# Performance work log

Hardware: AMD Instinct MI355X
Metric: run time of the kernel (lower is better)

## Reference

```python
import jax, jax.numpy as jnp
import numpy as np
import math

N_HEAD = 12

def alibi_slopes(h):
    x = (2 ** 8) ** (1.0 / h)
    return jnp.array([1.0 / x ** (i + 1) for i in range(h)], dtype=jnp.float32)

def setup_inputs() -> dict:
    key = jax.random.key(0)
    k0, k1, k2 = jax.random.split(key, 3)
    B, T, C = 4, 2048, 576
    x = jax.random.normal(k0, (B, T, C), dtype=jnp.float32)
    w_qkv = jax.random.normal(k1, (3 * C, C), dtype=jnp.float32) * 0.02
    w_proj = jax.random.normal(k2, (C, C), dtype=jnp.float32) * 0.02
    return {"x": x, "w_qkv": w_qkv, "w_proj": w_proj}

def reference(x, w_qkv, w_proj):
    B, T, C = x.shape
    H = N_HEAD
    D = C // H
    qkv = x @ w_qkv.T  # [B,T,3C]
    q, k, v = jnp.split(qkv, 3, axis=2)
    q = q.reshape(B, T, H, D).transpose(0, 2, 1, 3)  # [B,H,T,D]
    k = k.reshape(B, T, H, D).transpose(0, 2, 1, 3)
    v = v.reshape(B, T, H, D).transpose(0, 2, 1, 3)
    # value residual with v1=None: v = 0.5*v + 0.5*v = v (faithful no-op)
    scale = 1.0 / math.sqrt(D)
    att = jnp.einsum('bhid,bhjd->bhij', q, k) * scale  # [B,H,T,T]
    # ALiBi bias as written: (col - row).clamp(min=0) * slope (zero on causal part)
    col = jnp.arange(T, dtype=jnp.float32)[None, :]
    row = jnp.arange(T, dtype=jnp.float32)[:, None]
    bias = jnp.maximum(col - row, 0.0)[None, :, :] * alibi_slopes(H)[:, None, None]  # [H,T,T]
    att = att + bias[None]
    causal = (jnp.arange(T)[None, :] <= jnp.arange(T)[:, None])  # [T,T] lower-tri
    att = jnp.where(causal[None, None], att, -jnp.inf)
    att = jax.nn.softmax(att, axis=-1)
    y = jnp.einsum('bhij,bhjd->bhid', att, v)  # [B,H,T,D]
    y = y.transpose(0, 2, 1, 3).reshape(B, T, C)
    return y @ w_proj.T
```

## Files before the change

### kernel.cpp

```cpp
#include <hip/hip_runtime.h>
#include <math.h>

#define Bn 4
#define Tn 2048
#define Cn 576
#define Hn 12
#define Dn 48
#define Mn (Bn*Tn)

#define QSCALE (1.4426950408889634f * 0.14433756729740643f)

typedef short  short8  __attribute__((ext_vector_type(8)));
typedef float  floatx4 __attribute__((ext_vector_type(4)));
typedef unsigned short ushort_t;
typedef unsigned short ushort8_t __attribute__((ext_vector_type(8)));

static __device__ __forceinline__ unsigned short f2bf(float f) {
    union { float f; unsigned int u; } v; v.f = f;
    unsigned int r = v.u + 0x7FFFu + ((v.u >> 16) & 1u);
    return (unsigned short)(r >> 16);
}

static __device__ __forceinline__ unsigned int pack_trunc(float a, float b) {
    union { float f; unsigned int u; } ua, ub; ua.f = a; ub.f = b;
    return (ua.u >> 16) | (ub.u & 0xFFFF0000u);
}

static __device__ __forceinline__ void gload16(void* lds, const void* g) {
    __builtin_amdgcn_global_load_lds(
        (const __attribute__((address_space(1))) void*)g,
        (__attribute__((address_space(3))) void*)lds, 16, 0, 0);
}

template<int N> static __device__ __forceinline__ void vmgate() {
    if constexpr (N == 0)      asm volatile("s_waitcnt vmcnt(0)" ::: "memory");
    else if constexpr (N == 4) asm volatile("s_waitcnt vmcnt(4)" ::: "memory");
    else if constexpr (N == 8) asm volatile("s_waitcnt vmcnt(8)" ::: "memory");
}
static __device__ __forceinline__ void lgk0() {
    asm volatile("s_waitcnt lgkmcnt(0)" ::: "memory");
}
static __device__ __forceinline__ void barrier_fence() {
    asm volatile("" ::: "memory");
    __builtin_amdgcn_s_barrier();
    asm volatile("" ::: "memory");
}

template<int N> static __device__ __forceinline__ void wait_vm_lg() {
    if constexpr (N == 0)
        asm volatile("s_waitcnt vmcnt(0) lgkmcnt(0)" ::: "memory");
    else if constexpr (N == 3)
        asm volatile("s_waitcnt vmcnt(3) lgkmcnt(0)" ::: "memory");
    else if constexpr (N == 6)
        asm volatile("s_waitcnt vmcnt(6) lgkmcnt(0)" ::: "memory");
    else
        static_assert(N == -12345, "unsupported waitcnt immediate");
}

__global__ __launch_bounds__(256)
void cast3(const float* __restrict__ a, ushort_t* __restrict__ oa, int na4,
           const float* __restrict__ b, ushort_t* __restrict__ ob, int nb4,
           const float* __restrict__ c, ushort_t* __restrict__ oc, int nc4,
           ushort_t* __restrict__ zb)
{
    int i = blockIdx.x * 256 + threadIdx.x;
    if (blockIdx.x == 0 && threadIdx.x < 16) {
        float4 z = (float4){0.f, 0.f, 0.f, 0.f};
        ((float4*)zb)[threadIdx.x] = z;
    }
    const float* src; ushort_t* dst; int idx;
    if (i < na4)                  { src = a; dst = oa; idx = i; }
    else if (i < na4 + nb4)       { src = b; dst = ob; idx = i - na4; }
    else if (i < na4 + nb4 + nc4) { src = c; dst = oc; idx = i - na4 - nb4; }
    else return;
    float4 v = ((const float4*)src)[idx];
    ushort4 o;
    o.x = f2bf(v.x); o.y = f2bf(v.y); o.z = f2bf(v.z); o.w = f2bf(v.w);
    ((ushort4*)dst)[idx] = o;
}

__global__ __launch_bounds__(512)
void gemm_qkv(const ushort_t* __restrict__ A, const ushort_t* __restrict__ W,
              ushort_t* __restrict__ outb)
{
    __shared__ __align__(16) ushort_t Ls[8][8192];

    const int tid  = threadIdx.x;
    const int wave = tid >> 6;
    const int lane = tid & 63;
    const int m    = lane & 15;
    const int g    = lane >> 4;
    const int wr   = wave >> 2;
    const int wn   = wave & 3;

    const int bid  = blockIdx.x;
    const int xcd  = bid & 7;
    const int slot = bid >> 3;
    const int ng   = slot % 7;
    const int mg   = xcd + 8 * (slot / 7);
    const int m0   = mg * 256;
    const int n0g  = ng * 256;

    const int srow = lane >> 2;
    const int schk = (lane & 3) * 16;
    const char* aS0 = (const char*)A + (size_t)(m0  + (wave*2+0)*16 + srow) * (Cn*2) + schk;
    const char* aS1 = (const char*)A + (size_t)(m0  + (wave*2+1)*16 + srow) * (Cn*2) + schk;
    const char* bS0 = (const char*)W + (size_t)(n0g + (wave*2+0)*16 + srow) * (Cn*2) + schk;
    const char* bS1 = (const char*)W + (size_t)(n0g + (wave*2+1)*16 + srow) * (Cn*2) + schk;

    const int aoff = (wr * 128 + m) * 64 + g * 16;
    const int boff = (wn * 64  + m) * 64 + g * 16;

    floatx4 acc[8][4];
    #pragma unroll
    for (int i = 0; i < 8; ++i)
        #pragma unroll
        for (int j = 0; j < 4; ++j)
            acc[i][j] = (floatx4){0.f, 0.f, 0.f, 0.f};

    short8 af[8], bf01[2], bf23[2];

    auto stageA = [&](int s) {
        gload16(&Ls[s][(wave*2+0)*512], aS0); aS0 += 64;
        gload16(&Ls[s][(wave*2+1)*512], aS1); aS1 += 64;
    };
    auto stageB = [&](int s) {
        gload16(&Ls[s][(wave*2+0)*512], bS0); bS0 += 64;
        gload16(&Ls[s][(wave*2+1)*512], bS1); bS1 += 64;
    };
    auto loadA = [&](int s) {
        const char* base = (const char*)&Ls[s][0] + aoff;
        #pragma unroll
        for (int mf = 0; mf < 8; ++mf) af[mf] = *(const short8*)(base + mf * 1024);
    };
    auto loadB = [&](int s, int nf0, short8 (&bf)[2]) {
        const char* base = (const char*)&Ls[s][0] + boff;
        bf[0] = *(const short8*)(base + (nf0 + 0) * 1024);
        bf[1] = *(const short8*)(base + (nf0 + 1) * 1024);
    };
    auto mfma16 = [&](short8 (&bf)[2], int nf0) {
        __builtin_amdgcn_s_setprio(1);
        #pragma unroll
        for (int mf = 0; mf < 8; ++mf) {
            acc[mf][nf0]     = __builtin_amdgcn_mfma_f32_16x16x32_bf16(af[mf], bf[0], acc[mf][nf0],     0, 0, 0);
            acc[mf][nf0 + 1] = __builtin_amdgcn_mfma_f32_16x16x32_bf16(af[mf], bf[1], acc[mf][nf0 + 1], 0, 0, 0);
        }
        __builtin_amdgcn_s_setprio(0);
    };

    stageA(0); stageB(1); stageA(2); stageB(3); stageA(4); stageB(5);
    vmgate<8>();
    barrier_fence();

    #define QKV_TILE(s0, d0, d1, d2, d3, G1m, G3m) do {                         \
        constexpr int A0 = (s0) & 7,      B0 = ((s0)+1) & 7;                    \
        constexpr int A1 = ((s0)+2) & 7,  B1 = ((s0)+3) & 7;                    \
        constexpr int S0 = ((s0)+6) & 7,  S1 = ((s0)+7) & 7;                    \
        constexpr int S2 = ((s0)+8) & 7,  S3 = ((s0)+9) & 7;                    \
        loadA(A0); loadB(B0, 0, bf01);                                          \
        if (d0) stageA(S0);                                                     \
        barrier_fence(); lgk0();                                                \
        mfma16(bf01, 0);                                                        \
        barrier_fence();                                                        \
        loadB(B0, 2, bf23);                                                     \
        if (d1) stageB(S1);                                                     \
        barrier_fence(); lgk0();                                                \
        mfma16(bf23, 2);                                                        \
        vmgate<G1m>();                                                          \
        barrier_fence();                                                        \
        loadA(A1); loadB(B1, 0, bf01);                                          \
        if (d2) stageA(S2);                                                     \
        barrier_fence(); lgk0();                                                \
        mfma16(bf01, 0);                                                        \
        barrier_fence();                                                        \
        loadB(B1, 2, bf23);                                                     \
        if (d3) stageB(S3);                                                     \
        barrier_fence(); lgk0();                                                \
        mfma16(bf23, 2);                                                        \
        vmgate<G3m>();                                                          \
        barrier_fence();                                                        \
    } while (0)

    #pragma unroll 1
    for (int tt = 0; tt < 3; ++tt) {
        QKV_TILE(0, 1, 1, 1, 1, 8, 8);
        QKV_TILE(4, 1, 1, 1, 1, 8, 8);
    }
    QKV_TILE(0, 1, 1, 1, 1, 8, 8);
    QKV_TILE(4, 1, 1, 0, 0, 8, 4);
    QKV_TILE(0, 0, 0, 0, 0, 0, -1);
    #undef QKV_TILE

    const size_t per = (size_t)Bn * Hn * Tn * Dn;
    const int b  = m0 >> 11;
    const int t0 = m0 & 2047;
    ushort_t* Lc = (ushort_t*)&Ls[0][0];

    #pragma unroll
    for (int h2 = 0; h2 < 2; ++h2) {
        const int  nbase = n0g + h2 * 128;
        const bool vmode = (nbase >= 1152);
        if ((wn >> 1) == h2) {
            if (!vmode) {
                #pragma unroll
                for (int mf = 0; mf < 8; ++mf)
                    #pragma unroll
                    for (int nf = 0; nf < 4; ++nf) {
                        const int  nfb = n0g + wn * 64 + nf * 16;
                        const float sc = (nfb < 576) ? QSCALE : 1.0f;
                        const int col = (wn & 1) * 64 + nf * 16 + m;
                        const int rb  = wr * 128 + mf * 16 + g * 4;
                        #pragma unroll
                        for (int r = 0; r < 4; ++r)
                            Lc[(rb + r) * 136 + col] = f2bf(acc[mf][nf][r] * sc);
                    }
            } else {
                #pragma unroll
                for (int mf = 0; mf < 8; ++mf)
                    #pragma unroll
                    for (int nf = 0; nf < 4; ++nf) {
                        const int col = (wn & 1) * 64 + nf * 16 + m;
                        const int rb  = wr * 128 + mf * 16 + g * 4;
                        ushort4 pk;
                        pk.x = f2bf(acc[mf][nf][0]); pk.y = f2bf(acc[mf][nf][1]);
                        pk.z = f2bf(acc[mf][nf][2]); pk.w = f2bf(acc[mf][nf][3]);
                        *(ushort4*)&Lc[col * 264 + rb] = pk;
                    }
            }
        }
        __syncthreads();
        if (!vmode) {
            #pragma unroll
            for (int it = 0; it < 8; ++it) {
                const int c   = tid + it * 512;
                const int row = c >> 4;
                const int c8  = (c & 15) * 8;
                const int n   = nbase + c8;
                const int which = (n >= 576);
                const int nn  = n - which * 576;
                const int h   = nn / 48, d = nn - h * 48;
                ushort_t* dst = outb + (size_t)which * per
                    + ((size_t)(b * Hn + h) * Tn + t0 + row) * Dn + d;
                *(ushort8_t*)dst = *(const ushort8_t*)&Lc[row * 136 + c8];
            }
        } else {
            #pragma unroll
            for (int it = 0; it < 8; ++it) {
                const int c   = tid + it * 512;
                const int col = c >> 5;
                const int rc  = (c & 31) * 8;
                const int n   = nbase + col;
                if (n < 1728) {
                    const int dd = n - 1152;
                    const int h  = dd / 48, d = dd - h * 48;
                    ushort_t* dst = outb + 2 * per
                        + ((size_t)(b * Hn + h) * Dn + d) * Tn + t0 + rc;
                    *(ushort8_t*)dst = *(const ushort8_t*)&Lc[col * 264 + rc];
                }
            }
        }
        __syncthreads();
    }
}

template<int MODE, int MTILE>
__global__ __launch_bounds__(256)
void gemm_mfma(const ushort_t* __restrict__ A, const ushort_t* __restrict__ W,
               ushort_t* __restrict__ outb, float* __restrict__ outf)
{
    constexpr int SA   = MTILE / 16;
    constexpr int NSEG = SA + 4;
    constexpr int PW   = NSEG / 4;
    constexpr int MF   = MTILE / 64;
    constexpr int NB   = 9;
    constexpr int NST  = Cn / 32;
    constexpr int AH   = 3;
    constexpr int NBUF = 4;
    __shared__ __align__(16) ushort_t Ls[NBUF][NSEG][512];

    const int tid  = threadIdx.x;
    const int wave = tid >> 6;
    const int lane = tid & 63;
    const int m    = lane & 15;
    const int g    = lane >> 4;
    const int bid  = blockIdx.x;
    const int xcd  = bid & 7;
    const int slot = bid >> 3;
    const int n0   = (slot % NB) * 64;
    const int m0   = (xcd + 8 * (slot / NB)) * MTILE;

    floatx4 acc[MF][4];
    #pragma unroll
    for (int i = 0; i < MF; ++i)
        #pragma unroll
        for (int j = 0; j < 4; ++j)
            acc[i][j] = (floatx4){0.f, 0.f, 0.f, 0.f};

    const char* gp[PW];
    int         si[PW];
    #pragma unroll
    for (int i = 0; i < PW; ++i) {
        int s = wave + i * 4;
        si[i] = s;
        gp[i] = (s < SA)
            ? (const char*)(A + (size_t)(m0 + s * 16 + m) * Cn + g * 8)
            : (const char*)(W + (size_t)(n0 + (s - SA) * 16 + m) * Cn + g * 8);
    }

    #pragma unroll
    for (int s = 0; s < AH; ++s)
        #pragma unroll
        for (int i = 0; i < PW; ++i) { gload16(&Ls[s][si[i]][0], gp[i]); gp[i] += 64; }
    wait_vm_lg<(AH - 1) * PW>();
    __builtin_amdgcn_s_barrier();

    for (int j = 0; j < NST; ++j) {
        if (j + AH < NST) {
            #pragma unroll
            for (int i = 0; i < PW; ++i) {
                gload16(&Ls[(j + AH) & (NBUF - 1)][si[i]][0], gp[i]);
                gp[i] += 64;
            }
        }
        const int buf = j & (NBUF - 1);
        short8 bf4[4];
        #pragma unroll
        for (int jj = 0; jj < 4; ++jj)
            bf4[jj] = *(const short8*)&Ls[buf][SA + jj][lane * 8];
        #pragma unroll
        for (int i = 0; i < MF; ++i) {
            short8 afr = *(const short8*)&Ls[buf][wave * MF + i][lane * 8];
            #pragma unroll
            for (int jj = 0; jj < 4; ++jj)
                acc[i][jj] = __builtin_amdgcn_mfma_f32_16x16x32_bf16(afr, bf4[jj], acc[i][jj], 0, 0, 0);
        }
        if (j < NST - AH)        wait_vm_lg<(AH - 1) * PW>();
        else if (j == NST - AH)  wait_vm_lg<(AH - 2) * PW>();
        else                     wait_vm_lg<0>();
        __builtin_amdgcn_s_barrier();
    }

    #pragma unroll
    for (int i = 0; i < MF; ++i) {
        #pragma unroll
        for (int r = 0; r < 4; ++r) {
            int mrow = m0 + wave * (MTILE / 4) + i * 16 + g * 4 + r;
            #pragma unroll
            for (int j = 0; j < 4; ++j)
                outf[(size_t)mrow * Cn + n0 + j * 16 + m] = acc[i][j][r];
        }
    }
}

__global__ __launch_bounds__(512, 8)
void attn_mfma(const ushort_t* __restrict__ Q, const ushort_t* __restrict__ K,
               const ushort_t* __restrict__ V, ushort_t* __restrict__ Y,
               const ushort_t* __restrict__ zb)
{
    __shared__ __align__(16) ushort_t SMEM[20480];

    const int id   = blockIdx.x;
    const int kk   = id / 48;
    const int bh   = id - kk * 48;
    const int QT   = (kk & 1) ? (kk >> 1) : (15 - (kk >> 1));
    const int tid  = threadIdx.x;
    const int wave = tid >> 6;
    const int lane = tid & 63;
    const int m    = lane & 15;
    const int g    = lane >> 4;
    const int q0   = QT * 128;
    const int nkt  = 2 * QT + 2;

    const ushort_t* Qp = Q + (size_t)bh * Tn * Dn;
    const ushort_t* Kp = K + (size_t)bh * Tn * Dn;
    const ushort_t* Vp = V + (size_t)bh * Dn * Tn;

    {
        const char* qrp = (const char*)(Qp + (size_t)(q0 + wave * 16 + m) * Dn);
        gload16(&SMEM[(wave * 2 + 0) * 512], qrp + g * 16);
        gload16(&SMEM[(wave * 2 + 1) * 512], (g < 2) ? (qrp + 64 + g * 16) : (const char*)zb);
    }

    const char* kptr = (const char*)Kp + wave * 1024 + lane * 16;
    const int   vseg = wave - 2;
    const char* vptr = (const char*)(Vp + (size_t)((vseg >> 1) * 16 + m) * Tn)
                       + (vseg & 1) * 64 + g * 16;

    if (tid == 0) {
        ushort8_t z = (ushort8_t){0, 0, 0, 0, 0, 0, 0, 0};
        *(ushort8_t*)&SMEM[11264] = z;
        *(ushort8_t*)&SMEM[11272] = z;
    }

    if (wave < 6)  { gload16(&SMEM[8192 + wave * 512],  kptr); kptr += 6144; }
    if (wave >= 2) { gload16(&SMEM[14336 + vseg * 512], vptr); vptr += 128; }
    __syncthreads();

    short8 bq[2];
    bq[0] = *(const short8*)&SMEM[(wave * 2 + 0) * 512 + lane * 8];
    bq[1] = *(const short8*)&SMEM[(wave * 2 + 1) * 512 + lane * 8];

    floatx4 acc[3];
    #pragma unroll
    for (int t = 0; t < 3; ++t) acc[t] = (floatx4){0.f, 0.f, 0.f, 0.f};
    float l_tot = 0.f;
    const int qrow  = q0 + wave * 16 + m;
    const int qwmin = q0 + wave * 16;
    const int qwmax = qwmin + 15;
    const int koff  = m * 48 + g * 8;

    for (int jt = 0; jt < nkt; ++jt) {
        const int cur = jt & 1;
        const int j0  = jt * 64;
        if (jt + 1 < nkt) {
            if (wave < 6)  { gload16(&SMEM[8192 + (cur ^ 1) * 3072 + wave * 512],  kptr); kptr += 6144; }
            if (wave >= 2) { gload16(&SMEM[14336 + (cur ^ 1) * 3072 + vseg * 512], vptr); vptr += 128; }
        }

        if (j0 <= qwmax) {
            const ushort_t* Kb = &SMEM[8192 + cur * 3072 + koff];
            floatx4 s[4];
            #pragma unroll
            for (int t = 0; t < 4; ++t) {
                s[t] = (floatx4){0.f, 0.f, 0.f, 0.f};
                #pragma unroll
                for (int kc = 0; kc < 2; ++kc) {
                    short8 ak = *(const short8*)(Kb + t * 768 + kc * 32);
                    s[t] = __builtin_amdgcn_mfma_f32_16x16x32_bf16(ak, bq[kc], s[t], 0, 0, 0);
                }
            }

            float p[4][4];
            float lsum = 0.f;
            if (j0 + 63 > qwmin) {
                #pragma unroll
                for (int t = 0; t < 4; ++t)
                    #pragma unroll
                    for (int r = 0; r < 4; ++r) {
                        int j = j0 + t * 16 + g * 4 + r;
                        float v = (j <= qrow) ? s[t][r] : -1e30f;
                        float e = __builtin_amdgcn_exp2f(v);
                        p[t][r] = e; lsum += e;
                    }
            } else {
                #pragma unroll
                for (int t = 0; t < 4; ++t)
                    #pragma unroll
                    for (int r = 0; r < 4; ++r) {
                        float e = __builtin_amdgcn_exp2f(s[t][r]);
                        p[t][r] = e; lsum += e;
                    }
            }
            lsum += __shfl_xor(lsum, 16);
            lsum += __shfl_xor(lsum, 32);
            l_tot += lsum;

            #pragma unroll
            for (int t = 0; t < 4; ++t) {
                uint2 w2;
                w2.x = pack_trunc(p[t][0], p[t][1]);
                w2.y = pack_trunc(p[t][2], p[t][3]);
                *(uint2*)&SMEM[(wave * 2 + (t >> 1)) * 512
                               + (2 * (t & 1) + (g >> 1)) * 128 + m * 8 + (g & 1) * 4] = w2;
            }
            asm volatile("s_waitcnt lgkmcnt(0)" ::: "memory");

            #pragma unroll
            for (int kc = 0; kc < 2; ++kc) {
                short8 bp = *(const short8*)&SMEM[(wave * 2 + kc) * 512 + lane * 8];
                #pragma unroll
                for (int t = 0; t < 3; ++t) {
                    short8 av = *(const short8*)&SMEM[14336 + cur * 3072 + (t * 2 + kc) * 512 + lane * 8];
                    acc[t] = __builtin_amdgcn_mfma_f32_16x16x32_bf16(av, bp, acc[t], 0, 0, 0);
                }
            }
        }

        __syncthreads();
    }

    const float inv = 1.0f / l_tot;
    const int b = bh / Hn;
    const int h = bh - b * Hn;
    ushort_t* yp = Y + ((size_t)(b * Tn + qrow)) * Cn + h * Dn;
    #pragma unroll
    for (int t = 0; t < 3; ++t) {
        ushort4 o;
        o.x = f2bf(acc[t][0] * inv);
        o.y = f2bf(acc[t][1] * inv);
        o.z = f2bf(acc[t][2] * inv);
        o.w = f2bf(acc[t][3] * inv);
        *(ushort4*)&yp[t * 16 + g * 4] = o;
    }
}

extern "C" void kernel_launch(void* const* d_in, const int* in_sizes, int n_in,
                              void* d_out, int out_size, void* d_ws, size_t ws_size,
                              hipStream_t stream)
{
    const float* x      = (const float*)d_in[0];
    const float* w_qkv  = (const float*)d_in[1];
    const float* w_proj = (const float*)d_in[2];
    float* out = (float*)d_out;

    const size_t per = (size_t)Bn * Hn * Tn * Dn;

    ushort_t* xb  = (ushort_t*)d_ws;
    ushort_t* wqb = xb  + (size_t)Mn * Cn;
    ushort_t* wpb = wqb + (size_t)3 * Cn * Cn;
    ushort_t* qkv = wpb + (size_t)Cn * Cn;
    ushort_t* yb  = qkv + 3 * per;
    ushort_t* zb  = yb  + (size_t)Mn * Cn;

    const int na4 = Mn * Cn / 4, nb4 = 3 * Cn * Cn / 4, nc4 = Cn * Cn / 4;
    cast3<<<dim3((na4 + nb4 + nc4 + 255) / 256), dim3(256), 0, stream>>>(
        x, xb, na4, w_qkv, wqb, nb4, w_proj, wpb, nc4, zb);

    gemm_qkv<<<dim3(224), dim3(512), 0, stream>>>(xb, wqb, qkv);

    attn_mfma<<<dim3((Tn / 128) * Bn * Hn), dim3(512), 0, stream>>>(
        qkv, qkv + per, qkv + 2 * per, yb, zb);

    gemm_mfma<1, 128><<<dim3((Mn / 128) * 9), dim3(256), 0, stream>>>(yb, wpb, nullptr, out);
}
```

Baseline: 189.6 us.

## Triple-buffer K/V tiles in attention and shorten projection GEMM prefetch depth

The attention kernel moves from a double-buffered K/V staging scheme to a three-slot ring with two tiles in flight. It replaces the per-iteration __syncthreads with explicit vmcnt waits plus a barrier, so one load can stay outstanding across the barrier. This costs more LDS per block, and launch bounds drop from 8 to 6 blocks per CU. Separately, the projection GEMM drops from a 4-buffer/3-ahead pipeline to a 3-buffer/2-ahead ring with rotating indices, using less LDS at the price of less prefetch depth.

```diff
diff --git a/kernel.cpp b/kernel.cpp
--- a/kernel.cpp
+++ b/kernel.cpp
@@ -34,6 +34,8 @@
 
 template<int N> static __device__ __forceinline__ void vmgate() {
     if constexpr (N == 0)      asm volatile("s_waitcnt vmcnt(0)" ::: "memory");
+    else if constexpr (N == 1) asm volatile("s_waitcnt vmcnt(1)" ::: "memory");
+    else if constexpr (N == 2) asm volatile("s_waitcnt vmcnt(2)" ::: "memory");
     else if constexpr (N == 4) asm volatile("s_waitcnt vmcnt(4)" ::: "memory");
     else if constexpr (N == 8) asm volatile("s_waitcnt vmcnt(8)" ::: "memory");
 }
@@ -263,10 +265,10 @@
     }
 }
 
-template<int MODE, int MTILE>
+template<int MTILE>
 __global__ __launch_bounds__(256)
-void gemm_mfma(const ushort_t* __restrict__ A, const ushort_t* __restrict__ W,
-               ushort_t* __restrict__ outb, float* __restrict__ outf)
+void gemm_proj(const ushort_t* __restrict__ A, const ushort_t* __restrict__ W,
+               float* __restrict__ outf)
 {
     constexpr int SA   = MTILE / 16;
     constexpr int NSEG = SA + 4;
@@ -274,8 +276,8 @@
     constexpr int MF   = MTILE / 64;
     constexpr int NB   = 9;
     constexpr int NST  = Cn / 32;
-    constexpr int AH   = 3;
-    constexpr int NBUF = 4;
+    constexpr int AH   = 2;
+    constexpr int NBUF = 3;
     __shared__ __align__(16) ushort_t Ls[NBUF][NSEG][512];
 
     const int tid  = threadIdx.x;
@@ -314,15 +316,16 @@
     wait_vm_lg<(AH - 1) * PW>();
     __builtin_amdgcn_s_barrier();
 
+    int buf  = 0;
+    int sbuf = AH;
     for (int j = 0; j < NST; ++j) {
         if (j + AH < NST) {
             #pragma unroll
             for (int i = 0; i < PW; ++i) {
-                gload16(&Ls[(j + AH) & (NBUF - 1)][si[i]][0], gp[i]);
+                gload16(&Ls[sbuf][si[i]][0], gp[i]);
                 gp[i] += 64;
             }
         }
-        const int buf = j & (NBUF - 1);
         short8 bf4[4];
         #pragma unroll
         for (int jj = 0; jj < 4; ++jj)
@@ -334,10 +337,11 @@
             for (int jj = 0; jj < 4; ++jj)
                 acc[i][jj] = __builtin_amdgcn_mfma_f32_16x16x32_bf16(afr, bf4[jj], acc[i][jj], 0, 0, 0);
         }
-        if (j < NST - AH)        wait_vm_lg<(AH - 1) * PW>();
-        else if (j == NST - AH)  wait_vm_lg<(AH - 2) * PW>();
-        else                     wait_vm_lg<0>();
+        if (j < NST - AH) wait_vm_lg<(AH - 1) * PW>();
+        else              wait_vm_lg<0>();
         __builtin_amdgcn_s_barrier();
+        buf  = (buf  == NBUF - 1) ? 0 : buf  + 1;
+        sbuf = (sbuf == NBUF - 1) ? 0 : sbuf + 1;
     }
 
     #pragma unroll
@@ -352,12 +356,14 @@
     }
 }
 
-__global__ __launch_bounds__(512, 8)
+#define KS0 8192
+#define VS0 17408
+__global__ __launch_bounds__(512, 6)
 void attn_mfma(const ushort_t* __restrict__ Q, const ushort_t* __restrict__ K,
                const ushort_t* __restrict__ V, ushort_t* __restrict__ Y,
                const ushort_t* __restrict__ zb)
 {
-    __shared__ __align__(16) ushort_t SMEM[20480];
+    __shared__ __align__(16) ushort_t SMEM[26624];
 
     const int id   = blockIdx.x;
     const int kk   = id / 48;
@@ -375,6 +381,17 @@
     const ushort_t* Kp = K + (size_t)bh * Tn * Dn;
     const ushort_t* Vp = V + (size_t)bh * Dn * Tn;
 
+    const bool kw = (wave < 6);
+    const bool vw = (wave >= 2);
+    const int  vseg = wave - 2;
+
+    if (tid == 0) {
+        ushort8_t z = (ushort8_t){0, 0, 0, 0, 0, 0, 0, 0};
+        *(ushort8_t*)&SMEM[KS0 + 3072] = z;
+        *(ushort8_t*)&SMEM[KS0 + 6144] = z;
+    }
+    lgk0();
+
     {
         const char* qrp = (const char*)(Qp + (size_t)(q0 + wave * 16 + m) * Dn);
         gload16(&SMEM[(wave * 2 + 0) * 512], qrp + g * 16);
@@ -382,19 +399,15 @@
     }
 
     const char* kptr = (const char*)Kp + wave * 1024 + lane * 16;
-    const int   vseg = wave - 2;
     const char* vptr = (const char*)(Vp + (size_t)((vseg >> 1) * 16 + m) * Tn)
                        + (vseg & 1) * 64 + g * 16;
 
-    if (tid == 0) {
-        ushort8_t z = (ushort8_t){0, 0, 0, 0, 0, 0, 0, 0};
-        *(ushort8_t*)&SMEM[11264] = z;
-        *(ushort8_t*)&SMEM[11272] = z;
-    }
-
-    if (wave < 6)  { gload16(&SMEM[8192 + wave * 512],  kptr); kptr += 6144; }
-    if (wave >= 2) { gload16(&SMEM[14336 + vseg * 512], vptr); vptr += 128; }
-    __syncthreads();
+    if (kw) { gload16(&SMEM[KS0 + wave * 512],        kptr); kptr += 6144; }
+    if (vw) { gload16(&SMEM[VS0 + vseg * 512],        vptr); vptr += 128;  }
+    if (kw) { gload16(&SMEM[KS0 + 3072 + wave * 512], kptr); kptr += 6144; }
+    if (vw) { gload16(&SMEM[VS0 + 3072 + vseg * 512], vptr); vptr += 128;  }
+    if (kw && vw) vmgate<2>(); else vmgate<1>();
+    barrier_fence();
 
     short8 bq[2];
     bq[0] = *(const short8*)&SMEM[(wave * 2 + 0) * 512 + lane * 8];
@@ -409,16 +422,17 @@
     const int qwmax = qwmin + 15;
     const int koff  = m * 48 + g * 8;
 
+    int cb = 0;
+    int sb = 2;
     for (int jt = 0; jt < nkt; ++jt) {
-        const int cur = jt & 1;
-        const int j0  = jt * 64;
-        if (jt + 1 < nkt) {
-            if (wave < 6)  { gload16(&SMEM[8192 + (cur ^ 1) * 3072 + wave * 512],  kptr); kptr += 6144; }
-            if (wave >= 2) { gload16(&SMEM[14336 + (cur ^ 1) * 3072 + vseg * 512], vptr); vptr += 128; }
+        const int j0 = jt * 64;
+        if (jt + 2 < nkt) {
+            if (kw) { gload16(&SMEM[KS0 + sb * 3072 + wave * 512], kptr); kptr += 6144; }
+            if (vw) { gload16(&SMEM[VS0 + sb * 3072 + vseg * 512], vptr); vptr += 128;  }
         }
 
         if (j0 <= qwmax) {
-            const ushort_t* Kb = &SMEM[8192 + cur * 3072 + koff];
+            const ushort_t* Kb = &SMEM[KS0 + cb * 3072 + koff];
             floatx4 s[4];
             #pragma unroll
             for (int t = 0; t < 4; ++t) {
@@ -470,13 +484,20 @@
                 short8 bp = *(const short8*)&SMEM[(wave * 2 + kc) * 512 + lane * 8];
                 #pragma unroll
                 for (int t = 0; t < 3; ++t) {
-                    short8 av = *(const short8*)&SMEM[14336 + cur * 3072 + (t * 2 + kc) * 512 + lane * 8];
+                    short8 av = *(const short8*)&SMEM[VS0 + cb * 3072 + (t * 2 + kc) * 512 + lane * 8];
                     acc[t] = __builtin_amdgcn_mfma_f32_16x16x32_bf16(av, bp, acc[t], 0, 0, 0);
                 }
             }
         }
 
-        __syncthreads();
+        if (jt + 2 < nkt) {
+            if (kw && vw) vmgate<2>(); else vmgate<1>();
+        } else {
+            vmgate<0>();
+        }
+        barrier_fence();
+        cb = (cb == 2) ? 0 : cb + 1;
+        sb = (sb == 2) ? 0 : sb + 1;
     }
 
     const float inv = 1.0f / l_tot;
@@ -521,5 +542,5 @@
     attn_mfma<<<dim3((Tn / 128) * Bn * Hn), dim3(512), 0, stream>>>(
         qkv, qkv + per, qkv + 2 * per, yb, zb);
 
-    gemm_mfma<1, 128><<<dim3((Mn / 128) * 9), dim3(256), 0, stream>>>(yb, wpb, nullptr, out);
-}
+    gemm_proj<128><<<dim3((Mn / 128) * 9), dim3(256), 0, stream>>>(yb, wpb, out);
+}
```

Measured after the change: 164.2 us. 1.15x faster.
